# Performance work log

Hardware: AMD Instinct MI355X
Metric: run time of the kernel (lower is better)

## Reference

```python
import jax, jax.numpy as jnp
import numpy as np

IN_DIM = 512
MEM_DIM = 512
T = 256
B = 64


def _kaiming(key, shape):
    # kaiming_normal_ default: fan_in mode, gain sqrt(2)
    fan_in = shape[1]
    std = jnp.sqrt(2.0 / fan_in)
    return jax.random.normal(key, shape, dtype=jnp.float32) * std


def setup_inputs() -> dict:
    key = jax.random.key(0)
    ks = jax.random.split(key, 10)
    inp = {
        "inputs": jax.random.normal(ks[0], (T, B, IN_DIM), dtype=jnp.float32),
        "sememe_c": jax.random.normal(ks[1], (T, B, MEM_DIM), dtype=jnp.float32),
        "sememe_h": jax.random.normal(ks[2], (T, B, MEM_DIM), dtype=jnp.float32),
        "W_ioux": _kaiming(ks[3], (3 * MEM_DIM, IN_DIM)),
        "b_ioux": jnp.zeros((3 * MEM_DIM,), jnp.float32),
        "W_iouh": _kaiming(ks[4], (3 * MEM_DIM, MEM_DIM)),
        "b_iouh": jnp.zeros((3 * MEM_DIM,), jnp.float32),
        "W_ious": _kaiming(ks[5], (3 * MEM_DIM, MEM_DIM)),
        "b_ious": jnp.zeros((3 * MEM_DIM,), jnp.float32),
        "W_fx": _kaiming(ks[6], (MEM_DIM, IN_DIM)),
        "b_fx": jnp.zeros((MEM_DIM,), jnp.float32),
        "W_fxs": _kaiming(ks[7], (MEM_DIM, IN_DIM)),
        "b_fxs": jnp.zeros((MEM_DIM,), jnp.float32),
        "W_fh": _kaiming(ks[8], (MEM_DIM, MEM_DIM)),
        "b_fh": jnp.zeros((MEM_DIM,), jnp.float32),
        "W_fs": _kaiming(ks[9], (MEM_DIM, MEM_DIM)),
        "b_fs": jnp.zeros((MEM_DIM,), jnp.float32),
    }
    return inp


def reference(inputs, sememe_c, sememe_h,
              W_ioux, b_ioux, W_iouh, b_iouh, W_ious, b_ious,
              W_fx, b_fx, W_fxs, b_fxs, W_fh, b_fh, W_fs, b_fs):
    mem = W_fh.shape[0]
    batch = inputs.shape[1]

    # Precompute all input-dependent projections across time (parallel GEMMs).
    iou_x = jnp.einsum('tbi,gi->tbg', inputs, W_ioux) + b_ioux          # [T,B,3M]
    iou_s = jnp.einsum('tbm,gm->tbg', sememe_h, W_ious) + b_ious        # [T,B,3M]
    f_x = jnp.einsum('tbi,mi->tbm', inputs, W_fx) + b_fx                # [T,B,M]
    fs_pre = (jnp.einsum('tbi,mi->tbm', inputs, W_fxs) + b_fxs
              + jnp.einsum('tbm,nm->tbn', sememe_h, W_fs) + b_fs)       # [T,B,M]

    def step(carry, xs):
        c_prev, h_prev = carry
        iou_xs, f_xt, fs_t, sc_t = xs
        iou = iou_xs + h_prev @ W_iouh.T + b_iouh
        i = jax.nn.sigmoid(iou[:, :mem])
        o = jax.nn.sigmoid(iou[:, mem:2 * mem])
        u = jnp.tanh(iou[:, 2 * mem:])
        f = jax.nn.sigmoid(f_xt + h_prev @ W_fh.T + b_fh)
        f_s = jax.nn.sigmoid(fs_t)
        c = i * u + f * c_prev + f_s * sc_t
        h = o * jnp.tanh(c)
        return (c, h), h

    c0 = jnp.zeros((batch, mem), inputs.dtype)
    h0 = jnp.zeros((batch, mem), inputs.dtype)
    _, hs = jax.lax.scan(step, (c0, h0), (iou_x + iou_s, f_x, fs_pre, sememe_c))
    return hs  # [T,B,M]
```

## Files before the change

### kernel.cpp

```cpp
#include <hip/hip_runtime.h>


#define T_STEPS 256
#define BATCH   64
#define MEM     512
#define ROWS    16384

typedef __attribute__((ext_vector_type(8))) short bf16x8;
typedef __attribute__((ext_vector_type(4))) short short4v;
typedef __attribute__((ext_vector_type(4))) float f32x4;
typedef __attribute__((ext_vector_type(4))) unsigned int u32x4;

__device__ __forceinline__ short f2bf(float x) {
  unsigned u = __builtin_bit_cast(unsigned, x);
  u = u + 0x7fffu + ((u >> 16) & 1u);
  return (short)(u >> 16);
}
__device__ __forceinline__ float bf2f(short s) {
  unsigned u = ((unsigned)(unsigned short)s) << 16;
  return __builtin_bit_cast(float, u);
}
__device__ __forceinline__ float sigmoidf_(float x) { return 1.f / (1.f + expf(-x)); }

__device__ __forceinline__ u32x4 load16_sc(const void* p) {
  u32x4 r;
  asm volatile("global_load_dwordx4 %0, %1, off sc0 sc1" : "=v"(r) : "v"(p) : "memory");
  return r;
}
__device__ __forceinline__ void store4_sc(void* p, unsigned v) {
  asm volatile("global_store_dword %0, %1, off sc0 sc1" :: "v"(p), "v"(v) : "memory");
}
__device__ __forceinline__ unsigned poll4_sc(const void* p) {
  unsigned r;
  asm volatile("global_load_dword %0, %1, off sc0 sc1\ns_waitcnt vmcnt(0)"
               : "=v"(r) : "v"(p) : "memory");
  return r;
}

__global__ __launch_bounds__(256) void pack_act(
    const float* __restrict__ inputs, const float* __restrict__ sememe_h,
    char* __restrict__ Apack)
{
  int gid = blockIdx.x * 256 + threadIdx.x;
  int sel = gid >> 20;
  int rem = gid & 1048575;
  int R = rem >> 6, kg = rem & 63;
  const float* src = (sel ? sememe_h : inputs) + (size_t)R * 512 + kg * 8;
  float4 a = *(const float4*)src;
  float4 b = *(const float4*)(src + 4);
  float v[8] = {a.x, a.y, a.z, a.w, b.x, b.y, b.z, b.w};
  bf16x8 hi8, lo8;
#pragma unroll
  for (int e = 0; e < 8; ++e) {
    short h = f2bf(v[e]);
    hi8[e] = h;
    lo8[e] = f2bf(v[e] - bf2f(h));
  }
  int rt = R >> 7, r = R & 127, kt = sel * 16 + (kg >> 2), ls = kg & 3;
  char* rowp = Apack + ((size_t)((rt * 32 + kt) * 128 + r)) * 128;
  *(bf16x8*)(rowp + ((ls ^ (r & 7)) << 4))       = hi8;
  *(bf16x8*)(rowp + (((4 + ls) ^ (r & 7)) << 4)) = lo8;
}

__global__ __launch_bounds__(256) void pack_w(
    const float* __restrict__ W_ioux, const float* __restrict__ W_ious,
    const float* __restrict__ W_fx,   const float* __restrict__ W_fxs,
    const float* __restrict__ W_fs,   char* __restrict__ Wpack)
{
  int gid = blockIdx.x * 256 + threadIdx.x;
  if (gid >= 20 * 32 * 128 * 4) return;
  int ct = gid >> 14;
  int rem = gid & 16383;
  int ktv = rem >> 9;
  int rem2 = rem & 511;
  int cc = rem2 >> 2, kg = rem2 & 3;
  int region = (ct < 12) ? 0 : (ct < 16 ? 1 : 2);
  if (region == 1 && ktv >= 16) return;
  const float* srcrow;
  int k0;
  if (region == 0) {
    int c = ct * 128 + cc;
    if (ktv < 16) { srcrow = W_ioux + (size_t)c * 512; k0 = ktv * 32 + kg * 8; }
    else          { srcrow = W_ious + (size_t)c * 512; k0 = (ktv - 16) * 32 + kg * 8; }
  } else if (region == 1) {
    int c = (ct - 12) * 128 + cc;
    srcrow = W_fx + (size_t)c * 512; k0 = ktv * 32 + kg * 8;
  } else {
    int c = (ct - 16) * 128 + cc;
    if (ktv < 16) { srcrow = W_fxs + (size_t)c * 512; k0 = ktv * 32 + kg * 8; }
    else          { srcrow = W_fs  + (size_t)c * 512; k0 = (ktv - 16) * 32 + kg * 8; }
  }
  float4 a = *(const float4*)(srcrow + k0);
  float4 b = *(const float4*)(srcrow + k0 + 4);
  float v[8] = {a.x, a.y, a.z, a.w, b.x, b.y, b.z, b.w};
  bf16x8 hi8, lo8;
#pragma unroll
  for (int e = 0; e < 8; ++e) {
    short h = f2bf(v[e]);
    hi8[e] = h;
    lo8[e] = f2bf(v[e] - bf2f(h));
  }
  char* rowp = Wpack + ((size_t)((ct * 32 + ktv) * 128 + cc)) * 128;
  *(bf16x8*)(rowp + ((kg ^ (cc & 7)) << 4))       = hi8;
  *(bf16x8*)(rowp + (((4 + kg) ^ (cc & 7)) << 4)) = lo8;
}

#define GLL(gsrc, ldst) __builtin_amdgcn_global_load_lds( \
    (const __attribute__((address_space(1))) unsigned*)(gsrc), \
    (__attribute__((address_space(3))) unsigned*)(ldst), 16, 0, 0)

__global__ __launch_bounds__(256, 2) void gemm_mfma(
    const char* __restrict__ Apack, const char* __restrict__ Wpack,
    const float* __restrict__ sememe_c,
    const float* __restrict__ b_ioux, const float* __restrict__ b_iouh,
    const float* __restrict__ b_ious, const float* __restrict__ b_fx,
    const float* __restrict__ b_fh,  const float* __restrict__ b_fxs,
    const float* __restrict__ b_fs,
    float* __restrict__ iouT, float* __restrict__ fxT, float* __restrict__ fscT)
{
  __shared__ char ldsb[65536];
  __shared__ float bsum[128];

  const int bx = blockIdx.x;
  const int swz = (bx & 7) * 320 + (bx >> 3);
  const int rt = swz / 20, ct = swz % 20;
  const int tid = threadIdx.x, lane = tid & 63, wv = tid >> 6;
  const int wm = wv >> 1, wn = wv & 1;
  const int l15 = lane & 15, kgrp = lane >> 4;

  const int region = (ct < 12) ? 0 : (ct < 16 ? 1 : 2);
  const int cb0 = (region == 0) ? ct * 128 : (region == 1 ? (ct - 12) * 128 : (ct - 16) * 128);
  const int nkt = (region == 1) ? 16 : 32;

  if (tid < 128) {
    int c = cb0 + tid;
    bsum[tid] = (region == 0) ? b_ioux[c] + b_ious[c] + b_iouh[c]
              : (region == 1) ? b_fx[c] + b_fh[c]
                              : b_fxs[c] + b_fs[c];
  }

  const char* Ablk0 = Apack + (size_t)rt * 32 * 16384;
  const char* Wblk0 = Wpack + (size_t)ct * 32 * 16384;

  int aoffH[4], aoffL[4], boffH[4], boffL[4];
#pragma unroll
  for (int f = 0; f < 4; ++f) {
    int c_loc = wm * 64 + f * 16 + l15;
    aoffH[f] = c_loc * 128 + ((kgrp ^ (c_loc & 7)) << 4);
    aoffL[f] = c_loc * 128 + (((4 + kgrp) ^ (c_loc & 7)) << 4);
    int r_loc = wn * 64 + f * 16 + l15;
    boffH[f] = r_loc * 128 + ((kgrp ^ (r_loc & 7)) << 4);
    boffL[f] = r_loc * 128 + (((4 + kgrp) ^ (r_loc & 7)) << 4);
  }

#define STAGE(ktv, buf) do { \
    const char* As_ = Ablk0 + (size_t)(ktv) * 16384; \
    const char* Ws_ = Wblk0 + (size_t)(ktv) * 16384; \
    char* Ld_ = ldsb + (buf) * 32768; \
    _Pragma("unroll") \
    for (int i_ = 0; i_ < 4; ++i_) { \
      int off_ = (wv * 4 + i_) * 1024; \
      GLL(Ws_ + off_ + lane * 16, Ld_ + off_); \
      GLL(As_ + off_ + lane * 16, Ld_ + 16384 + off_); \
    } } while (0)

  f32x4 acc[4][4];
#pragma unroll
  for (int a = 0; a < 4; ++a)
#pragma unroll
    for (int b = 0; b < 4; ++b) acc[a][b] = (f32x4){0.f, 0.f, 0.f, 0.f};

  STAGE(0, 0);
  asm volatile("s_waitcnt vmcnt(0)" ::: "memory");
  __syncthreads();

  for (int kt = 0; kt < nkt; ++kt) {
    const int cur = kt & 1;
    if (kt + 1 < nkt) STAGE(kt + 1, cur ^ 1);
    const char* Wt = ldsb + cur * 32768;
    const char* At = Wt + 16384;
    bf16x8 AH[4], AL[4], BH[4], BL[4];
#pragma unroll
    for (int f = 0; f < 4; ++f) {
      AH[f] = *(const bf16x8*)(Wt + aoffH[f]);
      AL[f] = *(const bf16x8*)(Wt + aoffL[f]);
      BH[f] = *(const bf16x8*)(At + boffH[f]);
      BL[f] = *(const bf16x8*)(At + boffL[f]);
    }
#pragma unroll
    for (int fm = 0; fm < 4; ++fm)
#pragma unroll
      for (int fn = 0; fn < 4; ++fn) {
        acc[fm][fn] = __builtin_amdgcn_mfma_f32_16x16x32_bf16(AH[fm], BH[fn], acc[fm][fn], 0, 0, 0);
        acc[fm][fn] = __builtin_amdgcn_mfma_f32_16x16x32_bf16(AH[fm], BL[fn], acc[fm][fn], 0, 0, 0);
        acc[fm][fn] = __builtin_amdgcn_mfma_f32_16x16x32_bf16(AL[fm], BH[fn], acc[fm][fn], 0, 0, 0);
      }
    asm volatile("s_waitcnt vmcnt(0)" ::: "memory");
    __syncthreads();
  }

  const int r0 = rt * 128;
  float* stream = (region == 0) ? iouT : (region == 1) ? fxT : fscT;
#pragma unroll
  for (int fm = 0; fm < 4; ++fm)
#pragma unroll
    for (int fn = 0; fn < 4; ++fn) {
      int rr = r0 + wn * 64 + fn * 16 + l15;
#pragma unroll
      for (int i = 0; i < 4; ++i) {
        int c_loc = wm * 64 + fm * 16 + kgrp * 4 + i;
        float val = acc[fm][fn][i] + bsum[c_loc];
        if (region == 2)
          val = sigmoidf_(val) * sememe_c[(size_t)rr * MEM + cb0 + c_loc];
        stream[(size_t)(cb0 + c_loc) * ROWS + rr] = val;
      }
    }
}

__global__ __launch_bounds__(256, 1) void lstm_rec(
    const float* __restrict__ iouT,
    const float* __restrict__ fxT,
    const float* __restrict__ fscT,
    const float* __restrict__ W_iouh,
    const float* __restrict__ W_fh,
    unsigned* __restrict__ hplane,
    int* __restrict__ flags,
    float* __restrict__ out)
{
  const int wg = blockIdx.x, bg = wg >> 5, gm = wg & 31;
  const int m0 = gm * 16, B0 = bg * 16;
  const int tid = threadIdx.x, lane = tid & 63, wv = tid >> 6;

  const int arow = lane & 15, kgrp = lane >> 4;
  const float* wrow = (wv < 3) ? (W_iouh + (size_t)(wv * MEM + m0 + arow) * MEM)
                               : (W_fh   + (size_t)(m0 + arow) * MEM);
  bf16x8 Ahi[16], Alo[16];
#pragma unroll
  for (int kt = 0; kt < 16; ++kt) {
    const float* wp = wrow + kt * 32 + kgrp * 8;
    bf16x8 hi, lo;
#pragma unroll
    for (int e = 0; e < 8; ++e) {
      float w = wp[e];
      short h16 = f2bf(w);
      hi[e] = h16;
      lo[e] = f2bf(w - bf2f(h16));
    }
    Ahi[kt] = hi; Alo[kt] = lo;
  }

  __shared__ __align__(16) unsigned short BhiL[16][520];
  __shared__ __align__(16) unsigned short BloL[16][520];
  __shared__ float preLDS[16 * 68];
  __shared__ unsigned hT[16 * 17];

  unsigned* hg = hplane + (size_t)bg * 2 * 8192;
  int* flagp = flags + bg * 32;

  const int b8 = tid & 15, mj = tid >> 4;
  const int m = m0 + mj;
  const float* p_i = iouT + (size_t)m * ROWS;
  const float* p_o = iouT + (size_t)(MEM + m) * ROWS;
  const float* p_u = iouT + (size_t)(2 * MEM + m) * ROWS;
  const float* p_f = fxT  + (size_t)m * ROWS;
  const float* p_s = fscT + (size_t)m * ROWS;

  const int bb = lane & 15;
  float c_reg = 0.f;

  for (int t = 0; t < T_STEPS; ++t) {
    const int rb = t & 1;
    const int row = t * BATCH + B0 + b8;
    float ip = p_i[row], op = p_o[row], up = p_u[row], fp = p_f[row], sv = p_s[row];

    const unsigned* hPr = hg + (size_t)rb * 8192;
    u32x4 V[8];
#pragma unroll
    for (int i = 0; i < 8; ++i) V[i] = load16_sc(hPr + i * 1024 + tid * 4);
    asm volatile("s_waitcnt vmcnt(0)" ::: "memory");
    __builtin_amdgcn_sched_barrier(0);
#pragma unroll
    for (int i = 0; i < 8; ++i) {
      int d = i * 1024 + tid * 4;
      int b = d >> 9, mm = d & 511;
      u32x4 v = V[i];
      short4v hi4 = {(short)(v[0] >> 16), (short)(v[1] >> 16),
                     (short)(v[2] >> 16), (short)(v[3] >> 16)};
      short4v lo4 = {(short)(v[0] & 0xffff), (short)(v[1] & 0xffff),
                     (short)(v[2] & 0xffff), (short)(v[3] & 0xffff)};
      *(short4v*)&BhiL[b][mm] = hi4;
      *(short4v*)&BloL[b][mm] = lo4;
    }
    __syncthreads();

    f32x4 acc[4] = {{0.f,0.f,0.f,0.f},{0.f,0.f,0.f,0.f},{0.f,0.f,0.f,0.f},{0.f,0.f,0.f,0.f}};
#pragma unroll
    for (int kt = 0; kt < 16; ++kt) {
      bf16x8 bhiF = *(const bf16x8*)&BhiL[bb][kt * 32 + kgrp * 8];
      bf16x8 bloF = *(const bf16x8*)&BloL[bb][kt * 32 + kgrp * 8];
      acc[(3 * kt + 0) & 3] = __builtin_amdgcn_mfma_f32_16x16x32_bf16(Ahi[kt], bhiF, acc[(3 * kt + 0) & 3], 0, 0, 0);
      acc[(3 * kt + 1) & 3] = __builtin_amdgcn_mfma_f32_16x16x32_bf16(Ahi[kt], bloF, acc[(3 * kt + 1) & 3], 0, 0, 0);
      acc[(3 * kt + 2) & 3] = __builtin_amdgcn_mfma_f32_16x16x32_bf16(Alo[kt], bhiF, acc[(3 * kt + 2) & 3], 0, 0, 0);
    }
    f32x4 accs = (acc[0] + acc[1]) + (acc[2] + acc[3]);
#pragma unroll
    for (int i = 0; i < 4; ++i) preLDS[bb * 68 + wv * 16 + kgrp * 4 + i] = accs[i];
    __syncthreads();

    float pi = ip + preLDS[b8 * 68 + 0  + mj];
    float po = op + preLDS[b8 * 68 + 16 + mj];
    float pu = up + preLDS[b8 * 68 + 32 + mj];
    float pf = fp + preLDS[b8 * 68 + 48 + mj];
    float ig = sigmoidf_(pi);
    float og = sigmoidf_(po);
    float ug = tanhf(pu);
    float fg = sigmoidf_(pf);
    float cc = ig * ug + fg * c_reg + sv;
    float hv = og * tanhf(cc);
    c_reg = cc;
    out[(size_t)(t * BATCH + B0 + b8) * MEM + m] = hv;

    if (t == T_STEPS - 1) break;

    short h16 = f2bf(hv);
    short l16 = f2bf(hv - bf2f(h16));
    unsigned hu = ((unsigned)(unsigned short)h16 << 16) | (unsigned short)l16;
    hT[b8 * 17 + mj] = hu;
    __syncthreads();
    {
      int bs = tid >> 4, ms = tid & 15;
      unsigned v = hT[bs * 17 + ms];
      store4_sc(hg + (size_t)(rb ^ 1) * 8192 + bs * 512 + m0 + ms, v);
    }
    asm volatile("s_waitcnt vmcnt(0)" ::: "memory");
    __syncthreads();

    if (tid == 0) store4_sc(flagp + gm, (unsigned)(t + 1));
    if (wv == 0) {
      const int need = t + 1;
      int ok = (lane >= 32) ? 1 : 0;
      while (!__all(ok)) {
        if (!ok) ok = ((int)poll4_sc(flagp + (lane & 31)) >= need) ? 1 : 0;
      }
    }
    __syncthreads();
  }
}

extern "C" void kernel_launch(void* const* d_in, const int* in_sizes, int n_in,
                              void* d_out, int out_size, void* d_ws, size_t ws_size,
                              hipStream_t stream) {
  const float* inputs   = (const float*)d_in[0];
  const float* sememe_c = (const float*)d_in[1];
  const float* sememe_h = (const float*)d_in[2];
  const float* W_ioux   = (const float*)d_in[3];
  const float* b_ioux   = (const float*)d_in[4];
  const float* W_iouh   = (const float*)d_in[5];
  const float* b_iouh   = (const float*)d_in[6];
  const float* W_ious   = (const float*)d_in[7];
  const float* b_ious   = (const float*)d_in[8];
  const float* W_fx     = (const float*)d_in[9];
  const float* b_fx     = (const float*)d_in[10];
  const float* W_fxs    = (const float*)d_in[11];
  const float* b_fxs    = (const float*)d_in[12];
  const float* W_fh     = (const float*)d_in[13];
  const float* b_fh     = (const float*)d_in[14];
  const float* W_fs     = (const float*)d_in[15];
  const float* b_fs     = (const float*)d_in[16];

  float* iouT = (float*)d_ws;
  float* fxT  = iouT + (size_t)1536 * ROWS;
  float* fscT = fxT  + (size_t)512 * ROWS;
  char*  Apack = (char*)(fscT + (size_t)512 * ROWS);
  char*  Wpack = Apack + (size_t)128 * 32 * 128 * 128;
  unsigned* hplane = (unsigned*)(Wpack + (size_t)20 * 32 * 128 * 128);
  int* flags = (int*)(hplane + (size_t)4 * 2 * 8192);

  hipMemsetAsync(hplane, 0, (size_t)4 * 2 * 8192 * 4 + 512, stream);

  pack_act<<<dim3(8192), dim3(256), 0, stream>>>(inputs, sememe_h, Apack);
  pack_w<<<dim3(1280), dim3(256), 0, stream>>>(W_ioux, W_ious, W_fx, W_fxs, W_fs, Wpack);

  gemm_mfma<<<dim3(2560), dim3(256), 0, stream>>>(
      Apack, Wpack, sememe_c,
      b_ioux, b_iouh, b_ious, b_fx, b_fh, b_fxs, b_fs,
      iouT, fxT, fscT);

  lstm_rec<<<dim3(128), dim3(256), 0, stream>>>(
      iouT, fxT, fscT, W_iouh, W_fh, hplane, flags, (float*)d_out);
}
```

Measured before the change: 1.485 ms.

## Replace flag-based barrier with tagged h-plane polling and wider workgroups

Result: slower. 1.543 ms (+3.9%).

```diff
diff --git a/kernel.cpp b/kernel.cpp
--- a/kernel.cpp
+++ b/kernel.cpp
@@ -29,12 +29,6 @@
 }
 __device__ __forceinline__ void store4_sc(void* p, unsigned v) {
   asm volatile("global_store_dword %0, %1, off sc0 sc1" :: "v"(p), "v"(v) : "memory");
-}
-__device__ __forceinline__ unsigned poll4_sc(const void* p) {
-  unsigned r;
-  asm volatile("global_load_dword %0, %1, off sc0 sc1\ns_waitcnt vmcnt(0)"
-               : "=v"(r) : "v"(p) : "memory");
-  return r;
 }
 
 __global__ __launch_bounds__(256) void pack_act(
@@ -217,23 +211,24 @@
     }
 }
 
-__global__ __launch_bounds__(256, 1) void lstm_rec(
+__global__ __launch_bounds__(512, 1) void lstm_rec(
     const float* __restrict__ iouT,
     const float* __restrict__ fxT,
     const float* __restrict__ fscT,
     const float* __restrict__ W_iouh,
     const float* __restrict__ W_fh,
     unsigned* __restrict__ hplane,
-    int* __restrict__ flags,
     float* __restrict__ out)
 {
-  const int wg = blockIdx.x, bg = wg >> 5, gm = wg & 31;
-  const int m0 = gm * 16, B0 = bg * 16;
+  const int wg = blockIdx.x, bg = wg >> 4, gm = wg & 15;
+  const int m0 = gm * 32, B0 = bg * 16;
   const int tid = threadIdx.x, lane = tid & 63, wv = tid >> 6;
+  const int gate = wv & 3, half = wv >> 2;
 
   const int arow = lane & 15, kgrp = lane >> 4;
-  const float* wrow = (wv < 3) ? (W_iouh + (size_t)(wv * MEM + m0 + arow) * MEM)
-                               : (W_fh   + (size_t)(m0 + arow) * MEM);
+  const int mrow = m0 + half * 16 + arow;
+  const float* wrow = (gate < 3) ? (W_iouh + (size_t)(gate * MEM + mrow) * MEM)
+                                 : (W_fh   + (size_t)mrow * MEM);
   bf16x8 Ahi[16], Alo[16];
 #pragma unroll
   for (int kt = 0; kt < 16; ++kt) {
@@ -251,11 +246,11 @@
 
   __shared__ __align__(16) unsigned short BhiL[16][520];
   __shared__ __align__(16) unsigned short BloL[16][520];
-  __shared__ float preLDS[16 * 68];
-  __shared__ unsigned hT[16 * 17];
-
-  unsigned* hg = hplane + (size_t)bg * 2 * 8192;
-  int* flagp = flags + bg * 32;
+  __shared__ float preT[128 * 18];
+  __shared__ unsigned hT[16 * 33];
+  __shared__ int rdy[2][8];
+
+  unsigned* const hbase = hplane + (size_t)bg * 8192;
 
   const int b8 = tid & 15, mj = tid >> 4;
   const int m = m0 + mj;
@@ -265,31 +260,63 @@
   const float* p_f = fxT  + (size_t)m * ROWS;
   const float* p_s = fscT + (size_t)m * ROWS;
 
+  const int sb = tid >> 5;
+  const int smc = (tid & 31) * 16;
+  const bool ownSlice = (((tid & 31) >> 1) == gm);
+  const int ownOff = ((tid & 31) & 1) * 16;
+
   const int bb = lane & 15;
   float c_reg = 0.f;
 
   for (int t = 0; t < T_STEPS; ++t) {
     const int rb = t & 1;
+    const unsigned rtag = (unsigned)((t >> 1) & 1);
     const int row = t * BATCH + B0 + b8;
     float ip = p_i[row], op = p_o[row], up = p_u[row], fp = p_f[row], sv = p_s[row];
 
-    const unsigned* hPr = hg + (size_t)rb * 8192;
-    u32x4 V[8];
-#pragma unroll
-    for (int i = 0; i < 8; ++i) V[i] = load16_sc(hPr + i * 1024 + tid * 4);
-    asm volatile("s_waitcnt vmcnt(0)" ::: "memory");
-    __builtin_amdgcn_sched_barrier(0);
-#pragma unroll
-    for (int i = 0; i < 8; ++i) {
-      int d = i * 1024 + tid * 4;
-      int b = d >> 9, mm = d & 511;
-      u32x4 v = V[i];
-      short4v hi4 = {(short)(v[0] >> 16), (short)(v[1] >> 16),
-                     (short)(v[2] >> 16), (short)(v[3] >> 16)};
-      short4v lo4 = {(short)(v[0] & 0xffff), (short)(v[1] & 0xffff),
-                     (short)(v[2] & 0xffff), (short)(v[3] & 0xffff)};
-      *(short4v*)&BhiL[b][mm] = hi4;
-      *(short4v*)&BloL[b][mm] = lo4;
+    const unsigned* hPr = hbase + (size_t)rb * 32768;
+    u32x4 C[4];
+    int ok0, ok1, ok2, ok3;
+    if (ownSlice && t > 0) {
+#pragma unroll
+      for (int j = 0; j < 4; ++j)
+#pragma unroll
+        for (int d = 0; d < 4; ++d)
+          C[j][d] = hT[sb * 33 + ownOff + j * 4 + d];
+      ok0 = ok1 = ok2 = ok3 = 1;
+    } else {
+      ok0 = ok1 = ok2 = ok3 = 0;
+    }
+    int iterp = 0;
+    for (;;) {
+      if (!ok0) C[0] = load16_sc(hPr + tid * 16 + 0);
+      if (!ok1) C[1] = load16_sc(hPr + tid * 16 + 4);
+      if (!ok2) C[2] = load16_sc(hPr + tid * 16 + 8);
+      if (!ok3) C[3] = load16_sc(hPr + tid * 16 + 12);
+      asm volatile("s_waitcnt vmcnt(0)" ::: "memory");
+#define TAGOK(c) ((((c[0] ^ rtag) | (c[1] ^ rtag) | (c[2] ^ rtag) | (c[3] ^ rtag)) & 1u) == 0u)
+      ok0 = ok0 || TAGOK(C[0]);
+      ok1 = ok1 || TAGOK(C[1]);
+      ok2 = ok2 || TAGOK(C[2]);
+      ok3 = ok3 || TAGOK(C[3]);
+#undef TAGOK
+      int wall = __all(ok0 & ok1 & ok2 & ok3);
+      if (lane == 0) rdy[iterp][wv] = wall;
+      __syncthreads();
+      int g = rdy[iterp][0] & rdy[iterp][1] & rdy[iterp][2] & rdy[iterp][3] &
+              rdy[iterp][4] & rdy[iterp][5] & rdy[iterp][6] & rdy[iterp][7];
+      iterp ^= 1;
+      if (g) break;
+    }
+#pragma unroll
+    for (int j = 0; j < 4; ++j) {
+      u32x4 c = C[j];
+      short4v hi4 = {(short)(c[0] >> 16), (short)(c[1] >> 16),
+                     (short)(c[2] >> 16), (short)(c[3] >> 16)};
+      short4v lo4 = {(short)(c[0] & 0xffff), (short)(c[1] & 0xffff),
+                     (short)(c[2] & 0xffff), (short)(c[3] & 0xffff)};
+      *(short4v*)&BhiL[sb][smc + j * 4] = hi4;
+      *(short4v*)&BloL[sb][smc + j * 4] = lo4;
     }
     __syncthreads();
 
@@ -304,13 +331,14 @@
     }
     f32x4 accs = (acc[0] + acc[1]) + (acc[2] + acc[3]);
 #pragma unroll
-    for (int i = 0; i < 4; ++i) preLDS[bb * 68 + wv * 16 + kgrp * 4 + i] = accs[i];
+    for (int i = 0; i < 4; ++i)
+      preT[(gate * 32 + half * 16 + kgrp * 4 + i) * 18 + bb] = accs[i];
     __syncthreads();
 
-    float pi = ip + preLDS[b8 * 68 + 0  + mj];
-    float po = op + preLDS[b8 * 68 + 16 + mj];
-    float pu = up + preLDS[b8 * 68 + 32 + mj];
-    float pf = fp + preLDS[b8 * 68 + 48 + mj];
+    float pi = ip + preT[(0  + mj) * 18 + b8];
+    float po = op + preT[(32 + mj) * 18 + b8];
+    float pu = up + preT[(64 + mj) * 18 + b8];
+    float pf = fp + preT[(96 + mj) * 18 + b8];
     float ig = sigmoidf_(pi);
     float og = sigmoidf_(po);
     float ug = tanhf(pu);
@@ -318,32 +346,23 @@
     float cc = ig * ug + fg * c_reg + sv;
     float hv = og * tanhf(cc);
     c_reg = cc;
-    out[(size_t)(t * BATCH + B0 + b8) * MEM + m] = hv;
-
-    if (t == T_STEPS - 1) break;
-
-    short h16 = f2bf(hv);
-    short l16 = f2bf(hv - bf2f(h16));
-    unsigned hu = ((unsigned)(unsigned short)h16 << 16) | (unsigned short)l16;
-    hT[b8 * 17 + mj] = hu;
-    __syncthreads();
-    {
-      int bs = tid >> 4, ms = tid & 15;
-      unsigned v = hT[bs * 17 + ms];
-      store4_sc(hg + (size_t)(rb ^ 1) * 8192 + bs * 512 + m0 + ms, v);
-    }
-    asm volatile("s_waitcnt vmcnt(0)" ::: "memory");
-    __syncthreads();
-
-    if (tid == 0) store4_sc(flagp + gm, (unsigned)(t + 1));
-    if (wv == 0) {
-      const int need = t + 1;
-      int ok = (lane >= 32) ? 1 : 0;
-      while (!__all(ok)) {
-        if (!ok) ok = ((int)poll4_sc(flagp + (lane & 31)) >= need) ? 1 : 0;
+
+    if (t < T_STEPS - 1) {
+      const unsigned wtag = (unsigned)(((t + 1) >> 1) & 1);
+      short h16 = f2bf(hv);
+      short l16 = f2bf(hv - bf2f(h16));
+      unsigned hu = ((unsigned)(unsigned short)h16 << 16)
+                  | ((unsigned)(unsigned short)l16 & 0xFFFEu) | wtag;
+      hT[b8 * 33 + mj] = hu;
+      __syncthreads();
+      {
+        int psb = tid >> 5, psm = tid & 31;
+        unsigned v = hT[psb * 33 + psm];
+        unsigned* hPw = hbase + (size_t)(rb ^ 1) * 32768;
+        store4_sc(hPw + psb * 512 + m0 + psm, v);
       }
     }
-    __syncthreads();
+    out[(size_t)row * MEM + m] = hv;
   }
 }
 
@@ -374,9 +393,9 @@
   char*  Apack = (char*)(fscT + (size_t)512 * ROWS);
   char*  Wpack = Apack + (size_t)128 * 32 * 128 * 128;
   unsigned* hplane = (unsigned*)(Wpack + (size_t)20 * 32 * 128 * 128);
-  int* flags = (int*)(hplane + (size_t)4 * 2 * 8192);
-
-  hipMemsetAsync(hplane, 0, (size_t)4 * 2 * 8192 * 4 + 512, stream);
+
+  hipMemsetAsync(hplane,         0x00, 32768 * 4, stream);
+  hipMemsetAsync(hplane + 32768, 0x01, 32768 * 4, stream);
 
   pack_act<<<dim3(8192), dim3(256), 0, stream>>>(inputs, sememe_h, Apack);
   pack_w<<<dim3(1280), dim3(256), 0, stream>>>(W_ioux, W_ious, W_fx, W_fxs, W_fs, Wpack);
@@ -386,6 +405,6 @@
       b_ioux, b_iouh, b_ious, b_fx, b_fh, b_fxs, b_fs,
       iouT, fxT, fscT);
 
-  lstm_rec<<<dim3(128), dim3(256), 0, stream>>>(
-      iouT, fxT, fscT, W_iouh, W_fh, hplane, flags, (float*)d_out);
-}
+  lstm_rec<<<dim3(64), dim3(512), 0, stream>>>(
+      iouT, fxT, fscT, W_iouh, W_fh, hplane, (float*)d_out);
+}
```
